# Kernel optimization log

Hardware: AMD Instinct MI355X
Metric: run time of the kernel (lower is better)

## Reference

```python
import jax, jax.numpy as jnp
import numpy as np

N, E = 100000, 1600000
IN_D, HID, OUT_D = 64, 64, 16
BN_EPS = 1e-5


def setup_inputs() -> dict:
    key = jax.random.key(0)
    ks = list(jax.random.split(key, 32))
    k = iter(ks)
    inp = {}
    inp["x"] = jax.random.normal(next(k), (N, IN_D), dtype=jnp.float32)
    inp["edge_index"] = jax.random.randint(next(k), (2, E), 0, N, dtype=jnp.int64)
    def lin(kk, fan_in, fan_out):
        s = 1.0 / np.sqrt(fan_in)
        return jax.random.uniform(kk, (fan_in, fan_out), jnp.float32, -s, s)
    for i, ind in ((1, IN_D), (2, HID), (3, HID)):
        inp[f"eps{i}"] = jnp.zeros((), jnp.float32)
        inp[f"w{i}1"] = lin(next(k), ind, HID)
        inp[f"b{i}1"] = jnp.zeros((HID,), jnp.float32)
        inp[f"w{i}2"] = lin(next(k), HID, HID)
        inp[f"b{i}2"] = jnp.zeros((HID,), jnp.float32)
        inp[f"g{i}"] = jnp.ones((HID,), jnp.float32)
        inp[f"bt{i}"] = jnp.zeros((HID,), jnp.float32)
    inp["wl"] = lin(next(k), HID, OUT_D)
    inp["bl"] = jnp.zeros((OUT_D,), jnp.float32)
    return inp


def _gin_conv(x, src, dst, eps, w1, b1, w2, b2, g, bt):
    # scatter-add neighbor sum: agg[i] = sum_{(s->i) in E} x[s]
    agg = jax.ops.segment_sum(x[src], dst, num_segments=N)
    h = (1.0 + eps) * x + agg
    h = jax.nn.relu(h @ w1 + b1)
    h = jax.nn.relu(h @ w2 + b2)
    # BatchNorm1d over nodes (training mode: batch stats, biased variance)
    mu = jnp.mean(h, axis=0)
    var = jnp.var(h, axis=0)
    h = (h - mu) * jax.lax.rsqrt(var + BN_EPS) * g + bt
    return h


def reference(x, edge_index,
              eps1, w11, b11, w12, b12, g1, bt1,
              eps2, w21, b21, w22, b22, g2, bt2,
              eps3, w31, b31, w32, b32, g3, bt3,
              wl, bl):
    src, dst = edge_index[0], edge_index[1]
    h = jax.nn.relu(_gin_conv(x, src, dst, eps1, w11, b11, w12, b12, g1, bt1))
    h = jax.nn.relu(_gin_conv(h, src, dst, eps2, w21, b21, w22, b22, g2, bt2))
    h = jax.nn.relu(_gin_conv(h, src, dst, eps3, w31, b31, w32, b32, g3, bt3))
    return h @ wl + bl
```

## Files before the change

### kernel.cpp

```cpp
#include <hip/hip_runtime.h>
#include <hip/hip_fp16.h>
#include <math.h>

#define N_NODES 100000
#define N_PAD 100032
#define ROWS 32
#define NB 3125
#define NBLK64 1563
#define BN_EPS 1e-5f
#define PART_BLOCKS 128

typedef _Float16 half4v __attribute__((ext_vector_type(4)));
typedef float f32x4 __attribute__((ext_vector_type(4)));

__global__ void zero_misc_k(float* stats, int* gcnt) {
    int gid = blockIdx.x * blockDim.x + threadIdx.x;
    if (gid < 384) stats[gid] = 0.f;
    if (gid < NB) gcnt[gid] = 0;
}

__global__ void tofp16_k(const float* __restrict__ x, __half* __restrict__ xh, int n4) {
    int gid = blockIdx.x * blockDim.x + threadIdx.x;
    if (gid >= n4) return;
    float4 v = reinterpret_cast<const float4*>(x)[gid];
    union { float2 f; __half2 h[2]; } u;
    u.h[0] = __float22half2_rn(make_float2(v.x, v.y));
    u.h[1] = __float22half2_rn(make_float2(v.z, v.w));
    reinterpret_cast<float2*>(xh)[gid] = u.f;
}

__global__ void wtr_k(const float* w0, const float* w1, const float* w2,
                      const float* w3, const float* w4, const float* w5,
                      _Float16* wth) {
    const float* src[6] = {w0, w1, w2, w3, w4, w5};
    const float* W = src[blockIdx.x];
    _Float16* D = wth + (size_t)blockIdx.x * 4096;
    for (int idx = threadIdx.x; idx < 4096; idx += 256) {
        int k = idx >> 6, c = idx & 63;
        D[c * 64 + k] = (_Float16)W[idx];
    }
}

__global__ __launch_bounds__(256) void histA_k(const int* __restrict__ ei,
                                               int* __restrict__ gcnt, int E) {
    __shared__ int cnt[NB];
    for (int i = threadIdx.x; i < NB; i += 256) cnt[i] = 0;
    __syncthreads();
    int per = (E + gridDim.x - 1) / gridDim.x;
    int s0 = blockIdx.x * per, s1 = min(E, s0 + per);
    for (int e = s0 + threadIdx.x; e < s1; e += 256)
        atomicAdd(&cnt[ei[E + e] >> 5], 1);
    __syncthreads();
    for (int i = threadIdx.x; i < NB; i += 256)
        if (cnt[i]) atomicAdd(&gcnt[i], cnt[i]);
}

__global__ __launch_bounds__(256) void scanA_k(const int* __restrict__ gcnt,
                                               int* __restrict__ bbase,
                                               int* __restrict__ gcursor) {
    __shared__ int tmp[256];
    int t = threadIdx.x;
    int v[13];
    int s = 0;
#pragma unroll
    for (int j = 0; j < 13; ++j) {
        int idx = t * 13 + j;
        v[j] = (idx < NB) ? gcnt[idx] : 0;
        s += v[j];
    }
    tmp[t] = s;
    __syncthreads();
    for (int off = 1; off < 256; off <<= 1) {
        int a = (t >= off) ? tmp[t - off] : 0;
        __syncthreads();
        tmp[t] += a;
        __syncthreads();
    }
    int run = tmp[t] - s;
#pragma unroll
    for (int j = 0; j < 13; ++j) {
        int idx = t * 13 + j;
        if (idx < NB) { bbase[idx] = run; gcursor[idx] = run; }
        run += v[j];
    }
    if (t == 255) bbase[NB] = run;
}

__global__ __launch_bounds__(256) void partA_k(const int* __restrict__ ei,
                                               int* __restrict__ gcursor,
                                               int* __restrict__ part, int E) {
    __shared__ int cnt[NB];
    __shared__ int base[NB];
    for (int i = threadIdx.x; i < NB; i += 256) cnt[i] = 0;
    __syncthreads();
    int per = (E + gridDim.x - 1) / gridDim.x;
    int s0 = blockIdx.x * per, s1 = min(E, s0 + per);
    for (int e = s0 + threadIdx.x; e < s1; e += 256)
        atomicAdd(&cnt[ei[E + e] >> 5], 1);
    __syncthreads();
    for (int i = threadIdx.x; i < NB; i += 256) {
        int c = cnt[i];
        base[i] = c ? atomicAdd(&gcursor[i], c) : 0;
    }
    __syncthreads();
    for (int i = threadIdx.x; i < NB; i += 256) cnt[i] = 0;
    __syncthreads();
    for (int e = s0 + threadIdx.x; e < s1; e += 256) {
        int s = ei[e], d = ei[E + e];
        int b = d >> 5, dl = d & 31;
        int lo = atomicAdd(&cnt[b], 1);
        part[base[b] + lo] = (dl << 20) | s;
    }
}

__global__ __launch_bounds__(256) void sortB_k(const int* __restrict__ part,
                                               const int* __restrict__ bbase,
                                               int* __restrict__ row_ptr,
                                               int* __restrict__ csr_src) {
    __shared__ int cnt[ROWS];
    __shared__ int cur[ROWS];
    int b = blockIdx.x;
    int t = threadIdx.x;
    int e0 = bbase[b], e1 = bbase[b + 1];
    if (t < ROWS) cnt[t] = 0;
    __syncthreads();
    for (int i = e0 + t; i < e1; i += 256) atomicAdd(&cnt[(part[i] >> 20) & 31], 1);
    __syncthreads();
    if (t < ROWS) {
        int c = cnt[t];
        int v = c;
        for (int off = 1; off < ROWS; off <<= 1) {
            int u = __shfl_up(v, off, ROWS);
            if (t >= off) v += u;
        }
        int excl = v - c;
        row_ptr[b * ROWS + t] = e0 + excl;
        cur[t] = e0 + excl;
    }
    if (t == ROWS && b == NB - 1) row_ptr[N_NODES] = e1;
    __syncthreads();
    for (int i = e0 + t; i < e1; i += 256) {
        int u = part[i];
        int dl = (u >> 20) & 31;
        int pos = atomicAdd(&cur[dl], 1);
        csr_src[pos] = u & 0xFFFFF;
    }
}

__global__ __launch_bounds__(256) void gather_k(
    const __half* __restrict__ hin, const int* __restrict__ row_ptr,
    const int* __restrict__ csr_src, const float* __restrict__ epsp,
    __half* __restrict__ aggh) {
    int tid = threadIdx.x;
    int lg = tid >> 4, cg = tid & 15;
    int node = blockIdx.x * 16 + lg;
    float eps1 = 1.0f + *epsp;
    union F2H { float2 f; __half2 h[2]; };

    F2H sv;
    sv.f = reinterpret_cast<const float2*>(hin + (size_t)node * 64)[cg];
    float2 f0 = __half22float2(sv.h[0]);
    float2 f1 = __half22float2(sv.h[1]);
    float4 acc = make_float4(f0.x * eps1, f0.y * eps1, f1.x * eps1, f1.y * eps1);

    int j0 = row_ptr[node], j1 = row_ptr[node + 1];
    int j = j0;
    for (; j + 8 <= j1; j += 8) {
        int idx[8];
#pragma unroll
        for (int q = 0; q < 8; ++q) idx[q] = csr_src[j + q];
        F2H u[8];
#pragma unroll
        for (int q = 0; q < 8; ++q)
            u[q].f = reinterpret_cast<const float2*>(hin + (size_t)idx[q] * 64)[cg];
#pragma unroll
        for (int q = 0; q < 8; ++q) {
            float2 g0 = __half22float2(u[q].h[0]);
            float2 g1 = __half22float2(u[q].h[1]);
            acc.x += g0.x; acc.y += g0.y; acc.z += g1.x; acc.w += g1.y;
        }
    }
    for (; j < j1; ++j) {
        F2H u;
        u.f = reinterpret_cast<const float2*>(hin + (size_t)csr_src[j] * 64)[cg];
        float2 g0 = __half22float2(u.h[0]);
        float2 g1 = __half22float2(u.h[1]);
        acc.x += g0.x; acc.y += g0.y; acc.z += g1.x; acc.w += g1.y;
    }
    F2H o;
    o.h[0] = __float22half2_rn(make_float2(acc.x, acc.y));
    o.h[1] = __float22half2_rn(make_float2(acc.z, acc.w));
    reinterpret_cast<float2*>(aggh + (size_t)node * 64)[cg] = o.f;
}

__global__ __launch_bounds__(256) void mlp_k(
    const __half* __restrict__ aggh,
    const _Float16* __restrict__ wt1, const float* __restrict__ b1,
    const _Float16* __restrict__ wt2, const float* __restrict__ b2,
    __half* __restrict__ hout, float* __restrict__ stats) {
    __shared__ _Float16 hbuf[4][16][72];
    __shared__ float sred[128];

    int tid = threadIdx.x;
    int wid = tid >> 6, l = tid & 63;
    int c = l & 15, g = l >> 4;
    int r_base = blockIdx.x * 64 + wid * 16;

    if (tid < 128) sred[tid] = 0.f;
    __syncthreads();

    const _Float16* aggf = reinterpret_cast<const _Float16*>(aggh);

    half4v a1[4];
    {
        const _Float16* ab = aggf + (size_t)(r_base + c) * 64 + g * 4;
#pragma unroll
        for (int kk = 0; kk < 4; ++kk)
            a1[kk] = *reinterpret_cast<const half4v*>(ab + kk * 16);
    }

    f32x4 acc1[4];
#pragma unroll
    for (int n = 0; n < 4; ++n) {
        const _Float16* bb = wt1 + (size_t)(n * 16 + c) * 64 + g * 4;
        half4v bf[4];
#pragma unroll
        for (int kk = 0; kk < 4; ++kk)
            bf[kk] = *reinterpret_cast<const half4v*>(bb + kk * 16);
        f32x4 z = {0.f, 0.f, 0.f, 0.f};
#pragma unroll
        for (int kk = 0; kk < 4; ++kk)
            z = __builtin_amdgcn_mfma_f32_16x16x16f16(a1[kk], bf[kk], z, 0, 0, 0);
        acc1[n] = z;
    }

#pragma unroll
    for (int n = 0; n < 4; ++n) {
        float bj = b1[n * 16 + c];
#pragma unroll
        for (int e = 0; e < 4; ++e) {
            float v = fmaxf(acc1[n][e] + bj, 0.f);
            hbuf[wid][g * 4 + e][n * 16 + c] = (_Float16)v;
        }
    }

    half4v a2[4];
#pragma unroll
    for (int kk = 0; kk < 4; ++kk)
        a2[kk] = *reinterpret_cast<const half4v*>(&hbuf[wid][c][kk * 16 + g * 4]);

    f32x4 acc2[4];
#pragma unroll
    for (int n = 0; n < 4; ++n) {
        const _Float16* bb = wt2 + (size_t)(n * 16 + c) * 64 + g * 4;
        half4v bf[4];
#pragma unroll
        for (int kk = 0; kk < 4; ++kk)
            bf[kk] = *reinterpret_cast<const half4v*>(bb + kk * 16);
        f32x4 z = {0.f, 0.f, 0.f, 0.f};
#pragma unroll
        for (int kk = 0; kk < 4; ++kk)
            z = __builtin_amdgcn_mfma_f32_16x16x16f16(a2[kk], bf[kk], z, 0, 0, 0);
        acc2[n] = z;
    }

#pragma unroll
    for (int n = 0; n < 4; ++n) {
        float bj = b2[n * 16 + c];
        float s = 0.f, q = 0.f;
#pragma unroll
        for (int e = 0; e < 4; ++e) {
            float v = fmaxf(acc2[n][e] + bj, 0.f);
            hbuf[wid][g * 4 + e][n * 16 + c] = (_Float16)v;
            if (r_base + g * 4 + e < N_NODES) { s += v; q += v * v; }
        }
        atomicAdd(&sred[n * 16 + c], s);
        atomicAdd(&sred[64 + n * 16 + c], q);
    }

#pragma unroll
    for (int p = 0; p < 2; ++p) {
        int row = p * 8 + (l >> 3);
        int colh = (l & 7) * 8;
        int grow = r_base + row;
        if (grow < N_NODES) {
            float4 v = *reinterpret_cast<const float4*>(&hbuf[wid][row][colh]);
            *reinterpret_cast<float4*>(reinterpret_cast<__half*>(hout) +
                                       (size_t)grow * 64 + colh) = v;
        }
    }

    __syncthreads();
    if (tid < 128) atomicAdd(&stats[tid], sred[tid]);
}

__global__ __launch_bounds__(256) void bnrelu_k(const __half* hin,
                                                const float* __restrict__ stats,
                                                const float* __restrict__ g,
                                                const float* __restrict__ bt,
                                                __half* hout) {
    __shared__ float ssc[64], sof[64];
    int tid = threadIdx.x;
    if (tid < 64) {
        float mean = stats[tid] * (1.f / N_NODES);
        float var = stats[64 + tid] * (1.f / N_NODES) - mean * mean;
        float sc = g[tid] * rsqrtf(var + BN_EPS);
        ssc[tid] = sc;
        sof[tid] = bt[tid] - mean * sc;
    }
    __syncthreads();
    int gid = blockIdx.x * 256 + tid;
    if (gid >= N_NODES * 8) return;
    int c0 = (gid & 7) * 8;
    union { float4 f; __half2 h[4]; } u;
    u.f = reinterpret_cast<const float4*>(hin)[gid];
#pragma unroll
    for (int q = 0; q < 4; ++q) {
        float2 v = __half22float2(u.h[q]);
        v.x = fmaxf(fmaf(v.x, ssc[c0 + 2 * q], sof[c0 + 2 * q]), 0.f);
        v.y = fmaxf(fmaf(v.y, ssc[c0 + 2 * q + 1], sof[c0 + 2 * q + 1]), 0.f);
        u.h[q] = __float22half2_rn(v);
    }
    reinterpret_cast<float4*>(hout)[gid] = u.f;
}

__global__ __launch_bounds__(256) void final_k(const __half* __restrict__ hin,
                                               const float* __restrict__ wl,
                                               const float* __restrict__ bl,
                                               float* __restrict__ out) {
    __shared__ float xs[64][68];
    __shared__ float wsh[64 * 16];
    __shared__ float bsh[16];
    int tid = threadIdx.x;
    int r0 = blockIdx.x * 64;

    reinterpret_cast<float4*>(wsh)[tid] = reinterpret_cast<const float4*>(wl)[tid];
    if (tid < 16) bsh[tid] = bl[tid];

    {
        int rr = tid >> 4, cg = tid & 15;
#pragma unroll
        for (int i = 0; i < 4; ++i) {
            int r = rr + i * 16;
            float4 v = make_float4(0.f, 0.f, 0.f, 0.f);
            if (r0 + r < N_NODES) {
                union { float2 f; __half2 h[2]; } u;
                u.f = reinterpret_cast<const float2*>(hin + (size_t)(r0 + r) * 64)[cg];
                float2 f0 = __half22float2(u.h[0]);
                float2 f1 = __half22float2(u.h[1]);
                v = make_float4(f0.x, f0.y, f1.x, f1.y);
            }
            xs[cg * 4 + 0][r] = v.x;
            xs[cg * 4 + 1][r] = v.y;
            xs[cg * 4 + 2][r] = v.z;
            xs[cg * 4 + 3][r] = v.w;
        }
    }
    __syncthreads();

    int tc = tid & 3, r = tid >> 2;
    int c = tc * 4;
    float acc0 = 0.f, acc1 = 0.f, acc2 = 0.f, acc3 = 0.f;
#pragma unroll 8
    for (int k = 0; k < 64; ++k) {
        float xv = xs[k][r];
        float4 wv = *reinterpret_cast<const float4*>(&wsh[k * 16 + c]);
        acc0 = fmaf(xv, wv.x, acc0);
        acc1 = fmaf(xv, wv.y, acc1);
        acc2 = fmaf(xv, wv.z, acc2);
        acc3 = fmaf(xv, wv.w, acc3);
    }
    int row = r0 + r;
    if (row < N_NODES) {
        float4 o = make_float4(acc0 + bsh[c], acc1 + bsh[c + 1], acc2 + bsh[c + 2], acc3 + bsh[c + 3]);
        *reinterpret_cast<float4*>(out + (size_t)row * 16 + c) = o;
    }
}

extern "C" void kernel_launch(void* const* d_in, const int* in_sizes, int n_in,
                              void* d_out, int out_size, void* d_ws, size_t ws_size,
                              hipStream_t stream) {
    const float* x = (const float*)d_in[0];
    const int* ei = (const int*)d_in[1];
    const int E = in_sizes[1] / 2;

    const float* eps[3] = {(const float*)d_in[2], (const float*)d_in[9], (const float*)d_in[16]};
    const float* w1[3]  = {(const float*)d_in[3], (const float*)d_in[10], (const float*)d_in[17]};
    const float* b1[3]  = {(const float*)d_in[4], (const float*)d_in[11], (const float*)d_in[18]};
    const float* w2[3]  = {(const float*)d_in[5], (const float*)d_in[12], (const float*)d_in[19]};
    const float* b2[3]  = {(const float*)d_in[6], (const float*)d_in[13], (const float*)d_in[20]};
    const float* g[3]   = {(const float*)d_in[7], (const float*)d_in[14], (const float*)d_in[21]};
    const float* bt[3]  = {(const float*)d_in[8], (const float*)d_in[15], (const float*)d_in[22]};
    const float* wl = (const float*)d_in[23];
    const float* bl = (const float*)d_in[24];

    __half* xh   = (__half*)d_ws;
    __half* ha   = xh + (size_t)N_NODES * 64;
    __half* hb   = ha + (size_t)N_NODES * 64;
    __half* aggh = hb + (size_t)N_NODES * 64;
    _Float16* wth = (_Float16*)(aggh + (size_t)N_PAD * 64);
    float* stats = (float*)(wth + 6 * 4096);
    int* gcnt    = (int*)(stats + 384);
    int* bbase   = gcnt + NB;
    int* gcursor = bbase + (NB + 1);
    int* row_ptr = gcursor + NB;
    int* tail    = row_ptr + (N_NODES + 1);
    size_t used  = (size_t)((char*)tail - (char*)d_ws);

    int* csr_src = tail;
    int* part;
    if (used + 2 * (size_t)E * 4 <= ws_size) {
        part = csr_src + E;
    } else {
        part = (int*)d_out;
    }

    const int n4 = N_NODES * 16;

    zero_misc_k<<<(NB + 255) / 256, 256, 0, stream>>>(stats, gcnt);
    tofp16_k<<<(n4 + 255) / 256, 256, 0, stream>>>(x, xh, n4);
    wtr_k<<<6, 256, 0, stream>>>(w1[0], w2[0], w1[1], w2[1], w1[2], w2[2], wth);
    histA_k<<<PART_BLOCKS, 256, 0, stream>>>(ei, gcnt, E);
    scanA_k<<<1, 256, 0, stream>>>(gcnt, bbase, gcursor);
    partA_k<<<PART_BLOCKS, 256, 0, stream>>>(ei, gcursor, part, E);
    sortB_k<<<NB, 256, 0, stream>>>(part, bbase, row_ptr, csr_src);

    const int gthblk = N_NODES / 16;
    const int bnblk  = (N_NODES * 8 + 255) / 256;

    gather_k<<<gthblk, 256, 0, stream>>>(xh, row_ptr, csr_src, eps[0], aggh);
    mlp_k<<<NBLK64, 256, 0, stream>>>(aggh, wth + 0 * 4096, b1[0], wth + 1 * 4096, b2[0], ha, stats + 0);
    bnrelu_k<<<bnblk, 256, 0, stream>>>(ha, stats + 0, g[0], bt[0], ha);
    gather_k<<<gthblk, 256, 0, stream>>>(ha, row_ptr, csr_src, eps[1], aggh);
    mlp_k<<<NBLK64, 256, 0, stream>>>(aggh, wth + 2 * 4096, b1[1], wth + 3 * 4096, b2[1], hb, stats + 128);
    bnrelu_k<<<bnblk, 256, 0, stream>>>(hb, stats + 128, g[1], bt[1], hb);
    gather_k<<<gthblk, 256, 0, stream>>>(hb, row_ptr, csr_src, eps[2], aggh);
    mlp_k<<<NBLK64, 256, 0, stream>>>(aggh, wth + 4 * 4096, b1[2], wth + 5 * 4096, b2[2], ha, stats + 256);
    bnrelu_k<<<bnblk, 256, 0, stream>>>(ha, stats + 256, g[2], bt[2], ha);

    final_k<<<(N_NODES + 63) / 64, 256, 0, stream>>>(ha, wl, bl, (float*)d_out);
}
```

Baseline: 400.2 us.

## Fuse neighbor gather into MLP kernel and coarsen CSR bucket build

Merges the gather kernel into the per-layer MLP kernel, so each 64-row block aggregates neighbor features straight into shared memory and feeds them to the MFMA matmuls. This removes the fp16 aggregate buffer round trip through global memory and three kernel launches. The CSR build now uses 391 coarse buckets of 256 destination nodes instead of 3125 of 32, which shrinks the histogram, scan and partition shared arrays and replaces the second-pass warp scan with a block-wide scan. The fused kernel keeps all gather work on fewer threads per node row (4 rows per thread), which may lower memory-level parallelism for the irregular gather.

Measured after the change: 370.2 us. -7.5%, faster.

```diff
diff --git a/kernel.cpp b/kernel.cpp
--- a/kernel.cpp
+++ b/kernel.cpp
@@ -3,9 +3,7 @@
 #include <math.h>
 
 #define N_NODES 100000
-#define N_PAD 100032
-#define ROWS 32
-#define NB 3125
+#define NC 391
 #define NBLK64 1563
 #define BN_EPS 1e-5f
 #define PART_BLOCKS 128
@@ -16,7 +14,7 @@
 __global__ void zero_misc_k(float* stats, int* gcnt) {
     int gid = blockIdx.x * blockDim.x + threadIdx.x;
     if (gid < 384) stats[gid] = 0.f;
-    if (gid < NB) gcnt[gid] = 0;
+    if (gid < NC) gcnt[gid] = 0;
 }
 
 __global__ void tofp16_k(const float* __restrict__ x, __half* __restrict__ xh, int n4) {
@@ -41,33 +39,28 @@
     }
 }
 
-__global__ __launch_bounds__(256) void histA_k(const int* __restrict__ ei,
+__global__ __launch_bounds__(256) void histC_k(const int* __restrict__ ei,
                                                int* __restrict__ gcnt, int E) {
-    __shared__ int cnt[NB];
-    for (int i = threadIdx.x; i < NB; i += 256) cnt[i] = 0;
+    __shared__ int cnt[NC];
+    for (int i = threadIdx.x; i < NC; i += 256) cnt[i] = 0;
     __syncthreads();
     int per = (E + gridDim.x - 1) / gridDim.x;
     int s0 = blockIdx.x * per, s1 = min(E, s0 + per);
     for (int e = s0 + threadIdx.x; e < s1; e += 256)
-        atomicAdd(&cnt[ei[E + e] >> 5], 1);
-    __syncthreads();
-    for (int i = threadIdx.x; i < NB; i += 256)
+        atomicAdd(&cnt[ei[E + e] >> 8], 1);
+    __syncthreads();
+    for (int i = threadIdx.x; i < NC; i += 256)
         if (cnt[i]) atomicAdd(&gcnt[i], cnt[i]);
 }
 
-__global__ __launch_bounds__(256) void scanA_k(const int* __restrict__ gcnt,
-                                               int* __restrict__ bbase,
+__global__ __launch_bounds__(256) void scanC_k(const int* __restrict__ gcnt,
+                                               int* __restrict__ cbase,
                                                int* __restrict__ gcursor) {
     __shared__ int tmp[256];
     int t = threadIdx.x;
-    int v[13];
-    int s = 0;
-#pragma unroll
-    for (int j = 0; j < 13; ++j) {
-        int idx = t * 13 + j;
-        v[j] = (idx < NB) ? gcnt[idx] : 0;
-        s += v[j];
-    }
+    int v0 = (2 * t < NC) ? gcnt[2 * t] : 0;
+    int v1 = (2 * t + 1 < NC) ? gcnt[2 * t + 1] : 0;
+    int s = v0 + v1;
     tmp[t] = s;
     __syncthreads();
     for (int off = 1; off < 256; off <<= 1) {
@@ -77,147 +70,145 @@
         __syncthreads();
     }
     int run = tmp[t] - s;
-#pragma unroll
-    for (int j = 0; j < 13; ++j) {
-        int idx = t * 13 + j;
-        if (idx < NB) { bbase[idx] = run; gcursor[idx] = run; }
-        run += v[j];
-    }
-    if (t == 255) bbase[NB] = run;
-}
-
-__global__ __launch_bounds__(256) void partA_k(const int* __restrict__ ei,
+    if (2 * t < NC) { cbase[2 * t] = run; gcursor[2 * t] = run; }
+    run += v0;
+    if (2 * t + 1 < NC) { cbase[2 * t + 1] = run; gcursor[2 * t + 1] = run; }
+    if (t == 255) cbase[NC] = tmp[255];
+}
+
+__global__ __launch_bounds__(256) void partC_k(const int* __restrict__ ei,
                                                int* __restrict__ gcursor,
                                                int* __restrict__ part, int E) {
-    __shared__ int cnt[NB];
-    __shared__ int base[NB];
-    for (int i = threadIdx.x; i < NB; i += 256) cnt[i] = 0;
+    __shared__ int cnt[NC];
+    __shared__ int base[NC];
+    for (int i = threadIdx.x; i < NC; i += 256) cnt[i] = 0;
     __syncthreads();
     int per = (E + gridDim.x - 1) / gridDim.x;
     int s0 = blockIdx.x * per, s1 = min(E, s0 + per);
     for (int e = s0 + threadIdx.x; e < s1; e += 256)
-        atomicAdd(&cnt[ei[E + e] >> 5], 1);
-    __syncthreads();
-    for (int i = threadIdx.x; i < NB; i += 256) {
+        atomicAdd(&cnt[ei[E + e] >> 8], 1);
+    __syncthreads();
+    for (int i = threadIdx.x; i < NC; i += 256) {
         int c = cnt[i];
         base[i] = c ? atomicAdd(&gcursor[i], c) : 0;
     }
     __syncthreads();
-    for (int i = threadIdx.x; i < NB; i += 256) cnt[i] = 0;
+    for (int i = threadIdx.x; i < NC; i += 256) cnt[i] = 0;
     __syncthreads();
     for (int e = s0 + threadIdx.x; e < s1; e += 256) {
         int s = ei[e], d = ei[E + e];
-        int b = d >> 5, dl = d & 31;
+        int b = d >> 8, dl = d & 255;
         int lo = atomicAdd(&cnt[b], 1);
-        part[base[b] + lo] = (dl << 20) | s;
-    }
-}
-
-__global__ __launch_bounds__(256) void sortB_k(const int* __restrict__ part,
-                                               const int* __restrict__ bbase,
-                                               int* __restrict__ row_ptr,
-                                               int* __restrict__ csr_src) {
-    __shared__ int cnt[ROWS];
-    __shared__ int cur[ROWS];
+        part[base[b] + lo] = (dl << 17) | s;
+    }
+}
+
+__global__ __launch_bounds__(256) void csrD_k(const int* __restrict__ part,
+                                              const int* __restrict__ cbase,
+                                              int* __restrict__ row_ptr,
+                                              int* __restrict__ csr_src) {
+    __shared__ int cnt[256];
+    __shared__ int tmp[256];
+    __shared__ int cur[256];
     int b = blockIdx.x;
     int t = threadIdx.x;
-    int e0 = bbase[b], e1 = bbase[b + 1];
-    if (t < ROWS) cnt[t] = 0;
-    __syncthreads();
-    for (int i = e0 + t; i < e1; i += 256) atomicAdd(&cnt[(part[i] >> 20) & 31], 1);
-    __syncthreads();
-    if (t < ROWS) {
-        int c = cnt[t];
-        int v = c;
-        for (int off = 1; off < ROWS; off <<= 1) {
-            int u = __shfl_up(v, off, ROWS);
-            if (t >= off) v += u;
-        }
-        int excl = v - c;
-        row_ptr[b * ROWS + t] = e0 + excl;
-        cur[t] = e0 + excl;
-    }
-    if (t == ROWS && b == NB - 1) row_ptr[N_NODES] = e1;
+    int e0 = cbase[b], e1 = cbase[b + 1];
+    cnt[t] = 0;
+    __syncthreads();
+    for (int i = e0 + t; i < e1; i += 256) atomicAdd(&cnt[(part[i] >> 17) & 255], 1);
+    __syncthreads();
+    int c = cnt[t];
+    tmp[t] = c;
+    __syncthreads();
+    for (int off = 1; off < 256; off <<= 1) {
+        int a = (t >= off) ? tmp[t - off] : 0;
+        __syncthreads();
+        tmp[t] += a;
+        __syncthreads();
+    }
+    int excl = tmp[t] - c;
+    int node = b * 256 + t;
+    if (node < N_NODES) row_ptr[node] = e0 + excl;
+    cur[t] = e0 + excl;
     __syncthreads();
     for (int i = e0 + t; i < e1; i += 256) {
         int u = part[i];
-        int dl = (u >> 20) & 31;
+        int dl = (u >> 17) & 255;
         int pos = atomicAdd(&cur[dl], 1);
-        csr_src[pos] = u & 0xFFFFF;
-    }
-}
-
-__global__ __launch_bounds__(256) void gather_k(
-    const __half* __restrict__ hin, const int* __restrict__ row_ptr,
-    const int* __restrict__ csr_src, const float* __restrict__ epsp,
-    __half* __restrict__ aggh) {
-    int tid = threadIdx.x;
-    int lg = tid >> 4, cg = tid & 15;
-    int node = blockIdx.x * 16 + lg;
-    float eps1 = 1.0f + *epsp;
-    union F2H { float2 f; __half2 h[2]; };
-
-    F2H sv;
-    sv.f = reinterpret_cast<const float2*>(hin + (size_t)node * 64)[cg];
-    float2 f0 = __half22float2(sv.h[0]);
-    float2 f1 = __half22float2(sv.h[1]);
-    float4 acc = make_float4(f0.x * eps1, f0.y * eps1, f1.x * eps1, f1.y * eps1);
-
-    int j0 = row_ptr[node], j1 = row_ptr[node + 1];
-    int j = j0;
-    for (; j + 8 <= j1; j += 8) {
-        int idx[8];
-#pragma unroll
-        for (int q = 0; q < 8; ++q) idx[q] = csr_src[j + q];
-        F2H u[8];
-#pragma unroll
-        for (int q = 0; q < 8; ++q)
-            u[q].f = reinterpret_cast<const float2*>(hin + (size_t)idx[q] * 64)[cg];
-#pragma unroll
-        for (int q = 0; q < 8; ++q) {
-            float2 g0 = __half22float2(u[q].h[0]);
-            float2 g1 = __half22float2(u[q].h[1]);
-            acc.x += g0.x; acc.y += g0.y; acc.z += g1.x; acc.w += g1.y;
-        }
-    }
-    for (; j < j1; ++j) {
-        F2H u;
-        u.f = reinterpret_cast<const float2*>(hin + (size_t)csr_src[j] * 64)[cg];
-        float2 g0 = __half22float2(u.h[0]);
-        float2 g1 = __half22float2(u.h[1]);
-        acc.x += g0.x; acc.y += g0.y; acc.z += g1.x; acc.w += g1.y;
-    }
-    F2H o;
-    o.h[0] = __float22half2_rn(make_float2(acc.x, acc.y));
-    o.h[1] = __float22half2_rn(make_float2(acc.z, acc.w));
-    reinterpret_cast<float2*>(aggh + (size_t)node * 64)[cg] = o.f;
-}
-
-__global__ __launch_bounds__(256) void mlp_k(
-    const __half* __restrict__ aggh,
+        csr_src[pos] = u & 0x1FFFF;
+    }
+    if (b == NC - 1 && t == 0) row_ptr[N_NODES] = cbase[NC];
+}
+
+__global__ __launch_bounds__(256) void layer_k(
+    const __half* __restrict__ hin,
+    const int* __restrict__ row_ptr, const int* __restrict__ csr_src,
+    const float* __restrict__ epsp,
     const _Float16* __restrict__ wt1, const float* __restrict__ b1,
     const _Float16* __restrict__ wt2, const float* __restrict__ b2,
     __half* __restrict__ hout, float* __restrict__ stats) {
-    __shared__ _Float16 hbuf[4][16][72];
+    __shared__ _Float16 xs[64][72];
     __shared__ float sred[128];
 
     int tid = threadIdx.x;
+    int r0 = blockIdx.x * 64;
+    if (tid < 128) sred[tid] = 0.f;
+
+    float eps1 = 1.0f + *epsp;
+    int cg = tid & 15, lg = tid >> 4;
+    union F2H { float2 f; __half2 h[2]; };
+
+#pragma unroll
+    for (int i = 0; i < 4; ++i) {
+        int rloc = lg + i * 16;
+        int node = r0 + rloc;
+        float4 acc = make_float4(0.f, 0.f, 0.f, 0.f);
+        if (node < N_NODES) {
+            F2H sv;
+            sv.f = reinterpret_cast<const float2*>(hin + (size_t)node * 64)[cg];
+            float2 f0 = __half22float2(sv.h[0]);
+            float2 f1 = __half22float2(sv.h[1]);
+            acc = make_float4(f0.x * eps1, f0.y * eps1, f1.x * eps1, f1.y * eps1);
+            int j0 = row_ptr[node], j1 = row_ptr[node + 1];
+            int j = j0;
+            for (; j + 8 <= j1; j += 8) {
+                int idx[8];
+#pragma unroll
+                for (int q = 0; q < 8; ++q) idx[q] = csr_src[j + q];
+                F2H u[8];
+#pragma unroll
+                for (int q = 0; q < 8; ++q)
+                    u[q].f = reinterpret_cast<const float2*>(hin + (size_t)idx[q] * 64)[cg];
+#pragma unroll
+                for (int q = 0; q < 8; ++q) {
+                    float2 g0 = __half22float2(u[q].h[0]);
+                    float2 g1 = __half22float2(u[q].h[1]);
+                    acc.x += g0.x; acc.y += g0.y; acc.z += g1.x; acc.w += g1.y;
+                }
+            }
+            for (; j < j1; ++j) {
+                F2H u;
+                u.f = reinterpret_cast<const float2*>(hin + (size_t)csr_src[j] * 64)[cg];
+                float2 g0 = __half22float2(u.h[0]);
+                float2 g1 = __half22float2(u.h[1]);
+                acc.x += g0.x; acc.y += g0.y; acc.z += g1.x; acc.w += g1.y;
+            }
+        }
+        F2H o;
+        o.h[0] = __float22half2_rn(make_float2(acc.x, acc.y));
+        o.h[1] = __float22half2_rn(make_float2(acc.z, acc.w));
+        *reinterpret_cast<float2*>(&xs[rloc][cg * 4]) = o.f;
+    }
+    __syncthreads();
+
     int wid = tid >> 6, l = tid & 63;
     int c = l & 15, g = l >> 4;
-    int r_base = blockIdx.x * 64 + wid * 16;
-
-    if (tid < 128) sred[tid] = 0.f;
-    __syncthreads();
-
-    const _Float16* aggf = reinterpret_cast<const _Float16*>(aggh);
+    int r_base = r0 + wid * 16;
 
     half4v a1[4];
-    {
-        const _Float16* ab = aggf + (size_t)(r_base + c) * 64 + g * 4;
-#pragma unroll
-        for (int kk = 0; kk < 4; ++kk)
-            a1[kk] = *reinterpret_cast<const half4v*>(ab + kk * 16);
-    }
+#pragma unroll
+    for (int kk = 0; kk < 4; ++kk)
+        a1[kk] = *reinterpret_cast<const half4v*>(&xs[wid * 16 + c][g * 4 + kk * 16]);
 
     f32x4 acc1[4];
 #pragma unroll
@@ -240,14 +231,14 @@
 #pragma unroll
         for (int e = 0; e < 4; ++e) {
             float v = fmaxf(acc1[n][e] + bj, 0.f);
-            hbuf[wid][g * 4 + e][n * 16 + c] = (_Float16)v;
+            xs[wid * 16 + g * 4 + e][n * 16 + c] = (_Float16)v;
         }
     }
 
     half4v a2[4];
 #pragma unroll
     for (int kk = 0; kk < 4; ++kk)
-        a2[kk] = *reinterpret_cast<const half4v*>(&hbuf[wid][c][kk * 16 + g * 4]);
+        a2[kk] = *reinterpret_cast<const half4v*>(&xs[wid * 16 + c][kk * 16 + g * 4]);
 
     f32x4 acc2[4];
 #pragma unroll
@@ -271,7 +262,7 @@
 #pragma unroll
         for (int e = 0; e < 4; ++e) {
             float v = fmaxf(acc2[n][e] + bj, 0.f);
-            hbuf[wid][g * 4 + e][n * 16 + c] = (_Float16)v;
+            xs[wid * 16 + g * 4 + e][n * 16 + c] = (_Float16)v;
             if (r_base + g * 4 + e < N_NODES) { s += v; q += v * v; }
         }
         atomicAdd(&sred[n * 16 + c], s);
@@ -284,7 +275,7 @@
         int colh = (l & 7) * 8;
         int grow = r_base + row;
         if (grow < N_NODES) {
-            float4 v = *reinterpret_cast<const float4*>(&hbuf[wid][row][colh]);
+            float4 v = *reinterpret_cast<const float4*>(&xs[wid * 16 + row][colh]);
             *reinterpret_cast<float4*>(reinterpret_cast<__half*>(hout) +
                                        (size_t)grow * 64 + colh) = v;
         }
@@ -397,13 +388,12 @@
     __half* xh   = (__half*)d_ws;
     __half* ha   = xh + (size_t)N_NODES * 64;
     __half* hb   = ha + (size_t)N_NODES * 64;
-    __half* aggh = hb + (size_t)N_NODES * 64;
-    _Float16* wth = (_Float16*)(aggh + (size_t)N_PAD * 64);
+    _Float16* wth = (_Float16*)(hb + (size_t)N_NODES * 64);
     float* stats = (float*)(wth + 6 * 4096);
     int* gcnt    = (int*)(stats + 384);
-    int* bbase   = gcnt + NB;
-    int* gcursor = bbase + (NB + 1);
-    int* row_ptr = gcursor + NB;
+    int* cbase   = gcnt + NC;
+    int* gcursor = cbase + (NC + 1);
+    int* row_ptr = gcursor + NC;
     int* tail    = row_ptr + (N_NODES + 1);
     size_t used  = (size_t)((char*)tail - (char*)d_ws);
 
@@ -417,25 +407,29 @@
 
     const int n4 = N_NODES * 16;
 
-    zero_misc_k<<<(NB + 255) / 256, 256, 0, stream>>>(stats, gcnt);
+    zero_misc_k<<<2, 256, 0, stream>>>(stats, gcnt);
     tofp16_k<<<(n4 + 255) / 256, 256, 0, stream>>>(x, xh, n4);
     wtr_k<<<6, 256, 0, stream>>>(w1[0], w2[0], w1[1], w2[1], w1[2], w2[2], wth);
-    histA_k<<<PART_BLOCKS, 256, 0, stream>>>(ei, gcnt, E);
-    scanA_k<<<1, 256, 0, stream>>>(gcnt, bbase, gcursor);
-    partA_k<<<PART_BLOCKS, 256, 0, stream>>>(ei, gcursor, part, E);
-    sortB_k<<<NB, 256, 0, stream>>>(part, bbase, row_ptr, csr_src);
-
-    const int gthblk = N_NODES / 16;
-    const int bnblk  = (N_NODES * 8 + 255) / 256;
-
-    gather_k<<<gthblk, 256, 0, stream>>>(xh, row_ptr, csr_src, eps[0], aggh);
-    mlp_k<<<NBLK64, 256, 0, stream>>>(aggh, wth + 0 * 4096, b1[0], wth + 1 * 4096, b2[0], ha, stats + 0);
+    histC_k<<<PART_BLOCKS, 256, 0, stream>>>(ei, gcnt, E);
+    scanC_k<<<1, 256, 0, stream>>>(gcnt, cbase, gcursor);
+    partC_k<<<PART_BLOCKS, 256, 0, stream>>>(ei, gcursor, part, E);
+    csrD_k<<<NC, 256, 0, stream>>>(part, cbase, row_ptr, csr_src);
+
+    const int bnblk = (N_NODES * 8 + 255) / 256;
+
+    layer_k<<<NBLK64, 256, 0, stream>>>(xh, row_ptr, csr_src, eps[0],
+                                        wth + 0 * 4096, b1[0], wth + 1 * 4096, b2[0],
+                                        ha, stats + 0);
     bnrelu_k<<<bnblk, 256, 0, stream>>>(ha, stats + 0, g[0], bt[0], ha);
-    gather_k<<<gthblk, 256, 0, stream>>>(ha, row_ptr, csr_src, eps[1], aggh);
-    mlp_k<<<NBLK64, 256, 0, stream>>>(aggh, wth + 2 * 4096, b1[1], wth + 3 * 4096, b2[1], hb, stats + 128);
+
+    layer_k<<<NBLK64, 256, 0, stream>>>(ha, row_ptr, csr_src, eps[1],
+                                        wth + 2 * 4096, b1[1], wth + 3 * 4096, b2[1],
+                                        hb, stats + 128);
     bnrelu_k<<<bnblk, 256, 0, stream>>>(hb, stats + 128, g[1], bt[1], hb);
-    gather_k<<<gthblk, 256, 0, stream>>>(hb, row_ptr, csr_src, eps[2], aggh);
-    mlp_k<<<NBLK64, 256, 0, stream>>>(aggh, wth + 4 * 4096, b1[2], wth + 5 * 4096, b2[2], ha, stats + 256);
+
+    layer_k<<<NBLK64, 256, 0, stream>>>(hb, row_ptr, csr_src, eps[2],
+                                        wth + 4 * 4096, b1[2], wth + 5 * 4096, b2[2],
+                                        ha, stats + 256);
     bnrelu_k<<<bnblk, 256, 0, stream>>>(ha, stats + 256, g[2], bt[2], ha);
 
     final_k<<<(N_NODES + 63) / 64, 256, 0, stream>>>(ha, wl, bl, (float*)d_out);
```
